# Kernel optimization log

Hardware: AMD Instinct MI355X
Metric: run time of the kernel (lower is better)

The kernel has to match this reference:

```python
import jax, jax.numpy as jnp
import numpy as np

K = 3  # hardcoded in DRKNN.__init__


def setup_inputs() -> dict:
    key = jax.random.key(0)
    k1, k2, k3 = jax.random.split(key, 3)
    N, Q, A, B = 100000, 1024, 8, 16
    dataTensorX = jax.random.normal(k1, (N, A, B), dtype=jnp.float32)
    dataTensorY = jax.random.normal(k2, (N, 3), dtype=jnp.float32)
    inputTensor = jax.random.normal(k3, (Q, A, B), dtype=jnp.float32)
    return {"dataTensorX": dataTensorX, "dataTensorY": dataTensorY, "inputTensor": inputTensor}


def reference(dataTensorX, dataTensorY, inputTensor):
    # Flatten feature dims (1,2) -> single feature axis F = A*B
    N = dataTensorX.shape[0]
    Q = inputTensor.shape[0]
    X = dataTensorX.reshape(N, -1)   # [N, F]
    Qf = inputTensor.reshape(Q, -1)  # [Q, F]
    # squared L2 distance via expansion: ||q||^2 - 2 q.x + ||x||^2 -> [Q, N]
    x2 = jnp.sum(X * X, axis=-1)     # [N]
    q2 = jnp.sum(Qf * Qf, axis=-1)   # [Q]
    dists = q2[:, None] - 2.0 * (Qf @ X.T) + x2[None, :]  # [Q, N]
    # k smallest distances == k largest of negated distances
    _, idx = jax.lax.top_k(-dists, K)  # idx: [Q, K] int32
    outs = dataTensorY[idx]            # [Q, K, label_dim]
    out = jnp.mean(outs, axis=1)       # [Q, label_dim]
    return out, idx
```

## Files before the change

kernel.cpp:

```cpp
#include <hip/hip_runtime.h>

#define F       128
#define TILE    128
#define NCHUNKS 64
#define KSTEP   32
#define TOPK    3
#define DINF    (__builtin_inff())
#define IMAX    0x7fffffff

typedef short short8 __attribute__((ext_vector_type(8)));
typedef float f32x4  __attribute__((ext_vector_type(4)));

__device__ __forceinline__ ushort f2bf(float f) {
    uint u = __float_as_uint(f);
    uint r = (u + 0x7fffu + ((u >> 16) & 1u)) >> 16;
    return (ushort)r;
}

__device__ __forceinline__ bool lex_less(float d1, int i1, float d2, int i2) {
    return (d1 < d2) || (d1 == d2 && i1 < i2);
}

__device__ __forceinline__ int slotOf(int n, int g, int s) {
    int gg = g ^ ((n >> 2) & 3);
    int ss = s ^ (n & 3);
    return (n * 4 + gg) * 4 + ss;
}

__device__ __forceinline__ void loadRows(const ushort* __restrict__ src, uint4* v, int t) {
    const int n = t & 127, half = t >> 7;
    const uint4* s4 = reinterpret_cast<const uint4*>(src + (size_t)n * F + half * 64);
    #pragma unroll
    for (int c = 0; c < 8; c++) v[c] = s4[c];
}
__device__ __forceinline__ void writeLDS(const uint4* v, uint4* sX16, int t) {
    const int n = t & 127, half = t >> 7;
    const uint* u = reinterpret_cast<const uint*>(v);
    #pragma unroll
    for (int sp = 0; sp < 2; sp++)
        #pragma unroll
        for (int g = 0; g < 4; g++) {
            int c0 = sp * 4 + (g >> 1);
            int i0 = (g & 1) * 2;
            uint4 slot = make_uint4(u[c0 * 4 + i0], u[c0 * 4 + i0 + 1],
                                    u[(c0 + 2) * 4 + i0], u[(c0 + 2) * 4 + i0 + 1]);
            sX16[slotOf(n, g, half * 2 + sp)] = slot;
        }
}


__global__ void conv_kernel(const float* __restrict__ src, ushort* __restrict__ dst,
                            float* __restrict__ nrm, int rows, int rowsPad) {
    int row  = blockIdx.x * 4 + (threadIdx.x >> 6);
    int lane = threadIdx.x & 63;
    if (row >= rowsPad) return;
    if (row < rows) {
        float2 v = *reinterpret_cast<const float2*>(&src[(size_t)row * F + lane * 2]);
        ushort2 b; b.x = f2bf(v.x); b.y = f2bf(v.y);
        *reinterpret_cast<ushort2*>(&dst[(size_t)row * F + lane * 2]) = b;
        float s = v.x * v.x + v.y * v.y;
        #pragma unroll
        for (int m = 32; m >= 1; m >>= 1) s += __shfl_xor(s, m, 64);
        if (lane == 0) nrm[row] = s;
    } else {
        *reinterpret_cast<ushort2*>(&dst[(size_t)row * F + lane * 2]) = make_ushort2(0, 0);
        if (lane == 0) nrm[row] = DINF;
    }
}

__global__ __launch_bounds__(256) void knn_p1(
    const ushort* __restrict__ Xbf, const ushort* __restrict__ Qbf,
    const float* __restrict__ x2f, float* __restrict__ part,
    int NTILES, int NSUB)
{
    __shared__ uint4 sX16[2048];
    __shared__ float sx2[TILE];

    const int t   = threadIdx.x;
    const int w   = t >> 6;
    const int l   = t & 63;
    const int l15 = l & 15;
    const int g   = l >> 4;
    const int chunk = blockIdx.x;
    const int qbase = blockIdx.y * TILE;
    const int tile0 = (int)(((long)chunk * NTILES) >> 6);
    const int tile1 = (int)(((long)(chunk + 1) * NTILES) >> 6);

    {
        uint4 qv[8];
        loadRows(Qbf + (size_t)qbase * F, qv, t);
        writeLDS(qv, sX16, t);
    }
    __syncthreads();
    short8 qf[2][4];
    #pragma unroll
    for (int fqi = 0; fqi < 2; fqi++)
        #pragma unroll
        for (int s = 0; s < 4; s++) {
            int qn = w * 32 + fqi * 16 + l15;
            qf[fqi][s] = *reinterpret_cast<const short8*>(&sX16[slotOf(qn, g, s)]);
        }

    uint4 v[8];
    loadRows(Xbf + (size_t)tile0 * TILE * F, v, t);

    for (int tile = tile0; tile < tile1; tile++) {
        __syncthreads();
        writeLDS(v, sX16, t);
        if (t < 32)
            *reinterpret_cast<float4*>(&sx2[t * 4]) =
                *reinterpret_cast<const float4*>(&x2f[tile * TILE + t * 4]);
        if (tile + 1 < tile1)
            loadRows(Xbf + (size_t)(tile + 1) * TILE * F, v, t);
        __syncthreads();

        f32x4 acc[8][2];
        #pragma unroll
        for (int fm = 0; fm < 8; fm++)
            #pragma unroll
            for (int fqi = 0; fqi < 2; fqi++)
                acc[fm][fqi] = (f32x4){0.f, 0.f, 0.f, 0.f};

        #pragma unroll
        for (int s = 0; s < 4; s++) {
            short8 af[8];
            #pragma unroll
            for (int fm = 0; fm < 8; fm++)
                af[fm] = *reinterpret_cast<const short8*>(&sX16[slotOf(fm * 16 + l15, g, s)]);
            #pragma unroll
            for (int fm = 0; fm < 8; fm++) {
                acc[fm][0] = __builtin_amdgcn_mfma_f32_16x16x32_bf16(af[fm], qf[0][s], acc[fm][0], 0, 0, 0);
                acc[fm][1] = __builtin_amdgcn_mfma_f32_16x16x32_bf16(af[fm], qf[1][s], acc[fm][1], 0, 0, 0);
            }
        }

        #pragma unroll
        for (int sb = 0; sb < 4; sb++) {
            float4 xa = *reinterpret_cast<const float4*>(&sx2[sb * 32 + g * 4]);
            float4 xb = *reinterpret_cast<const float4*>(&sx2[sb * 32 + 16 + g * 4]);
            #pragma unroll
            for (int fqi = 0; fqi < 2; fqi++) {
                f32x4 ca = acc[sb * 2][fqi];
                f32x4 cb = acc[sb * 2 + 1][fqi];
                float t0 = fmaf(-2.f, ca[0], xa.x), t1 = fmaf(-2.f, ca[1], xa.y);
                float t2 = fmaf(-2.f, ca[2], xa.z), t3 = fmaf(-2.f, ca[3], xa.w);
                float t4 = fmaf(-2.f, cb[0], xb.x), t5 = fmaf(-2.f, cb[1], xb.y);
                float t6 = fmaf(-2.f, cb[2], xb.z), t7 = fmaf(-2.f, cb[3], xb.w);
                float m = fminf(fminf(fminf(t0, t1), fminf(t2, t3)),
                                fminf(fminf(t4, t5), fminf(t6, t7)));
                m = fminf(m, __shfl_xor(m, 16, 64));
                m = fminf(m, __shfl_xor(m, 32, 64));
                if (g == 0)
                    part[(size_t)(qbase + w * 32 + fqi * 16 + l15) * NSUB + (tile * 4 + sb)] = m;
            }
        }
    }
}

__global__ __launch_bounds__(256) void knn_p2(
    const float* __restrict__ part, const float* __restrict__ Xf,
    const float* __restrict__ x2f, const float* __restrict__ Qf,
    const float* __restrict__ q2f, const float* __restrict__ Y,
    float* __restrict__ out, int NSUB, int qTotal, int Nreal)
{
    __shared__ float sq[4][F];
    __shared__ int   scnt[4];
    __shared__ int   slist[4][128];

    const int t = threadIdx.x, w = t >> 6, l = t & 63;
    const int q = blockIdx.x * 4 + w;

    *reinterpret_cast<float2*>(&sq[w][l * 2]) =
        *reinterpret_cast<const float2*>(&Qf[(size_t)q * F + l * 2]);
    if (l == 0) scnt[w] = 0;
    __syncthreads();

    const float q2v = q2f[q];
    const int iters = (NSUB + 63) / 64;
    const size_t prow = (size_t)q * NSUB;

    float a0 = DINF, a1 = DINF, a2 = DINF;
    for (int it = 0; it < iters; it++) {
        int i = it * 64 + l;
        float v = (i < NSUB) ? part[prow + i] : DINF;
        if (v < a2) { a2 = v;
            if (a2 < a1) { float x = a2; a2 = a1; a1 = x; }
            if (a1 < a0) { float x = a1; a1 = a0; a0 = x; } }
    }
    #pragma unroll
    for (int m = 1; m < 64; m <<= 1) {
        float o0 = __shfl_xor(a0, m, 64), o1 = __shfl_xor(a1, m, 64), o2 = __shfl_xor(a2, m, 64);
        #pragma unroll
        for (int c = 0; c < 3; c++) {
            float v = (c == 0) ? o0 : (c == 1) ? o1 : o2;
            if (v < a2) { a2 = v;
                if (a2 < a1) { float x = a2; a2 = a1; a1 = x; }
                if (a1 < a0) { float x = a1; a1 = a0; a0 = x; } }
        }
    }
    const float tau = a2 + 4.5f;

    for (int it = 0; it < iters; it++) {
        int i = it * 64 + l;
        float v = (i < NSUB) ? part[prow + i] : DINF;
        if (v <= tau) {
            int slot = atomicAdd(&scnt[w], 1);
            if (slot < 128) slist[w][slot] = i;
        }
    }
    __syncthreads();
    const int ncand = min(scnt[w], 128);

    float b0d = DINF, b1d = DINF, b2d = DINF;
    int   b0i = IMAX, b1i = IMAX, b2i = IMAX;
    auto ins = [&](float d, int ix) {
        if (lex_less(d, ix, b2d, b2i)) {
            b2d = d; b2i = ix;
            if (lex_less(b2d, b2i, b1d, b1i)) {
                float td = b2d; b2d = b1d; b1d = td; int ti = b2i; b2i = b1i; b1i = ti; }
            if (lex_less(b1d, b1i, b0d, b0i)) {
                float td = b1d; b1d = b0d; b0d = td; int ti = b1i; b1i = b0i; b0i = ti; }
        }
    };

    const int half = l >> 5, pl = l & 31;
    for (int ci = 0; ci < ncand; ci++) {
        int p = slist[w][ci] * 32 + pl;
        float s = 0.f;
        if (p < Nreal) {
            const float4* xr = reinterpret_cast<const float4*>(&Xf[(size_t)p * F + half * 64]);
            const float4* qr = reinterpret_cast<const float4*>(&sq[w][half * 64]);
            float s0 = 0.f, s1 = 0.f, s2 = 0.f, s3 = 0.f;
            #pragma unroll
            for (int j = 0; j < 16; j++) {
                float4 xv = xr[j], qv = qr[j];
                s0 = fmaf(xv.x, qv.x, s0); s1 = fmaf(xv.y, qv.y, s1);
                s2 = fmaf(xv.z, qv.z, s2); s3 = fmaf(xv.w, qv.w, s3);
            }
            s = (s0 + s1) + (s2 + s3);
        }
        s += __shfl_xor(s, 32, 64);
        if (l < 32 && p < Nreal) {
            float d = (q2v - 2.0f * s) + x2f[p];
            ins(d, p);
        }
    }

    #pragma unroll
    for (int m = 1; m < 64; m <<= 1) {
        float od0 = __shfl_xor(b0d, m, 64); int oi0 = __shfl_xor(b0i, m, 64);
        float od1 = __shfl_xor(b1d, m, 64); int oi1 = __shfl_xor(b1i, m, 64);
        float od2 = __shfl_xor(b2d, m, 64); int oi2 = __shfl_xor(b2i, m, 64);
        ins(od0, oi0); ins(od1, oi1); ins(od2, oi2);
    }

    if (l == 0) {
        int idx_off = qTotal * 3;
        #pragma unroll
        for (int c = 0; c < 3; c++) {
            float s = Y[(size_t)b0i * 3 + c] + Y[(size_t)b1i * 3 + c] + Y[(size_t)b2i * 3 + c];
            out[q * 3 + c] = s / 3.0f;
        }
        out[idx_off + q * 3 + 0] = (float)b0i;
        out[idx_off + q * 3 + 1] = (float)b1i;
        out[idx_off + q * 3 + 2] = (float)b2i;
    }
}


__global__ void fb_rownorm(const float* __restrict__ src, float* __restrict__ dst, int rows) {
    int row  = blockIdx.x * 4 + (threadIdx.x >> 6);
    int lane = threadIdx.x & 63;
    if (row >= rows) return;
    float2 v = *reinterpret_cast<const float2*>(&src[(size_t)row * F + lane * 2]);
    float s = v.x * v.x + v.y * v.y;
    #pragma unroll
    for (int m = 32; m >= 1; m >>= 1) s += __shfl_xor(s, m, 64);
    if (lane == 0) dst[row] = s;
}

__global__ __launch_bounds__(256) void fb_phase1(
    const float* __restrict__ X, const float* __restrict__ Qm,
    const float* __restrict__ x2, const float* __restrict__ q2,
    float* __restrict__ part_d, int* __restrict__ part_i,
    int N, int ntiles)
{
    __shared__ __align__(16) union {
        struct { float a[KSTEP * TILE]; float b[KSTEP * TILE]; } s;
        struct { float d[TILE][16][TOPK]; int i[TILE][16][TOPK]; } r;
    } u;

    const int t  = threadIdx.x;
    const int tx = t & 15;
    const int ty = t >> 4;
    const int chunk = blockIdx.x;
    const int qbase = blockIdx.y * TILE;
    const int ar0 = ty * 4;
    const int bc0 = tx * 4;
    const int srow0 = t >> 2;
    const int skc0  = t & 3;

    float t3d[8][TOPK];
    int   t3i[8][TOPK];
    #pragma unroll
    for (int i = 0; i < 8; i++)
        #pragma unroll
        for (int c = 0; c < TOPK; c++) { t3d[i][c] = DINF; t3i[i][c] = IMAX; }

    float q2r[8];
    #pragma unroll
    for (int i = 0; i < 8; i++) {
        int r = (i < 4) ? (ar0 + i) : (64 + ar0 + i - 4);
        q2r[i] = q2[qbase + r];
    }

    for (int tile = chunk; tile < ntiles; tile += NCHUNKS) {
        float acc[8][8];
        #pragma unroll
        for (int i = 0; i < 8; i++)
            #pragma unroll
            for (int j = 0; j < 8; j++) acc[i][j] = 0.0f;

        for (int ks = 0; ks < F; ks += KSTEP) {
            __syncthreads();
            #pragma unroll
            for (int lq = 0; lq < 4; lq++) {
                int row = srow0 | ((lq >> 1) << 6);
                int kc  = skc0 | ((lq & 1) << 2);
                int sw  = (kc & 3) << 3;
                int base = (kc * 4) * TILE + (row ^ sw);

                float4 va = *reinterpret_cast<const float4*>(
                    &Qm[(size_t)(qbase + row) * F + ks + kc * 4]);
                u.s.a[base + 0 * TILE] = va.x;
                u.s.a[base + 1 * TILE] = va.y;
                u.s.a[base + 2 * TILE] = va.z;
                u.s.a[base + 3 * TILE] = va.w;

                int n = tile * TILE + row;
                float4 vb = make_float4(0.f, 0.f, 0.f, 0.f);
                if (n < N) vb = *reinterpret_cast<const float4*>(
                    &X[(size_t)n * F + ks + kc * 4]);
                u.s.b[base + 0 * TILE] = vb.x;
                u.s.b[base + 1 * TILE] = vb.y;
                u.s.b[base + 2 * TILE] = vb.z;
                u.s.b[base + 3 * TILE] = vb.w;
            }
            __syncthreads();

            #pragma unroll
            for (int kk = 0; kk < KSTEP; kk++) {
                int sw = ((kk >> 2) & 3) << 3;
                float4 a0 = *reinterpret_cast<const float4*>(&u.s.a[kk * TILE + (ar0 ^ sw)]);
                float4 a1 = *reinterpret_cast<const float4*>(&u.s.a[kk * TILE + 64 + (ar0 ^ sw)]);
                float4 b0 = *reinterpret_cast<const float4*>(&u.s.b[kk * TILE + (bc0 ^ sw)]);
                float4 b1 = *reinterpret_cast<const float4*>(&u.s.b[kk * TILE + 64 + (bc0 ^ sw)]);
                float av[8] = {a0.x, a0.y, a0.z, a0.w, a1.x, a1.y, a1.z, a1.w};
                float bv[8] = {b0.x, b0.y, b0.z, b0.w, b1.x, b1.y, b1.z, b1.w};
                #pragma unroll
                for (int i = 0; i < 8; i++)
                    #pragma unroll
                    for (int j = 0; j < 8; j++)
                        acc[i][j] = fmaf(av[i], bv[j], acc[i][j]);
            }
        }

        #pragma unroll
        for (int j = 0; j < 8; j++) {
            int n = tile * TILE + ((j < 4) ? (bc0 + j) : (64 + bc0 + j - 4));
            if (n < N) {
                float xc = x2[n];
                #pragma unroll
                for (int i = 0; i < 8; i++) {
                    float d = (q2r[i] - 2.0f * acc[i][j]) + xc;
                    if (d < t3d[i][2]) {
                        t3d[i][2] = d; t3i[i][2] = n;
                        if (t3d[i][2] < t3d[i][1]) {
                            float td = t3d[i][2]; t3d[i][2] = t3d[i][1]; t3d[i][1] = td;
                            int ti = t3i[i][2]; t3i[i][2] = t3i[i][1]; t3i[i][1] = ti;
                        }
                        if (t3d[i][1] < t3d[i][0]) {
                            float td = t3d[i][1]; t3d[i][1] = t3d[i][0]; t3d[i][0] = td;
                            int ti = t3i[i][1]; t3i[i][1] = t3i[i][0]; t3i[i][0] = ti;
                        }
                    }
                }
            }
        }
    }

    __syncthreads();
    #pragma unroll
    for (int i = 0; i < 8; i++) {
        int r = (i < 4) ? (ar0 + i) : (64 + ar0 + i - 4);
        #pragma unroll
        for (int c = 0; c < TOPK; c++) {
            u.r.d[r][tx][c] = t3d[i][c];
            u.r.i[r][tx][c] = t3i[i][c];
        }
    }
    __syncthreads();

    if (t < TILE) {
        int row = t;
        float b0d = DINF, b1d = DINF, b2d = DINF;
        int   b0i = IMAX, b1i = IMAX, b2i = IMAX;
        for (int s = 0; s < 16; s++) {
            #pragma unroll
            for (int c = 0; c < TOPK; c++) {
                float d = u.r.d[row][s][c];
                int  ix = u.r.i[row][s][c];
                if (lex_less(d, ix, b2d, b2i)) {
                    b2d = d; b2i = ix;
                    if (lex_less(b2d, b2i, b1d, b1i)) {
                        float td = b2d; b2d = b1d; b1d = td;
                        int ti = b2i; b2i = b1i; b1i = ti;
                    }
                    if (lex_less(b1d, b1i, b0d, b0i)) {
                        float td = b1d; b1d = b0d; b0d = td;
                        int ti = b1i; b1i = b0i; b0i = ti;
                    }
                }
            }
        }
        size_t base = ((size_t)(qbase + row) * NCHUNKS + chunk) * TOPK;
        part_d[base + 0] = b0d; part_d[base + 1] = b1d; part_d[base + 2] = b2d;
        part_i[base + 0] = b0i; part_i[base + 1] = b1i; part_i[base + 2] = b2i;
    }
}

__global__ void fb_phase2(const float* __restrict__ part_d, const int* __restrict__ part_i,
                          const float* __restrict__ Y, float* __restrict__ out, int Q)
{
    int q    = blockIdx.x * 4 + (threadIdx.x >> 6);
    int lane = threadIdx.x & 63;
    if (q >= Q) return;

    float b0d = DINF, b1d = DINF, b2d = DINF;
    int   b0i = IMAX, b1i = IMAX, b2i = IMAX;

    auto ins = [&](float d, int ix) {
        if (lex_less(d, ix, b2d, b2i)) {
            b2d = d; b2i = ix;
            if (lex_less(b2d, b2i, b1d, b1i)) {
                float td = b2d; b2d = b1d; b1d = td;
                int ti = b2i; b2i = b1i; b1i = ti;
            }
            if (lex_less(b1d, b1i, b0d, b0i)) {
                float td = b1d; b1d = b0d; b0d = td;
                int ti = b1i; b1i = b0i; b0i = ti;
            }
        }
    };

    const int total = NCHUNKS * TOPK;
    size_t base = (size_t)q * total;
    for (int e = lane; e < total; e += 64)
        ins(part_d[base + e], part_i[base + e]);

    #pragma unroll
    for (int m = 1; m < 64; m <<= 1) {
        float od0 = __shfl_xor(b0d, m, 64); int oi0 = __shfl_xor(b0i, m, 64);
        float od1 = __shfl_xor(b1d, m, 64); int oi1 = __shfl_xor(b1i, m, 64);
        float od2 = __shfl_xor(b2d, m, 64); int oi2 = __shfl_xor(b2i, m, 64);
        ins(od0, oi0); ins(od1, oi1); ins(od2, oi2);
    }

    if (lane == 0) {
        int idx_off = Q * 3;
        #pragma unroll
        for (int c = 0; c < 3; c++) {
            float s = Y[(size_t)b0i * 3 + c] + Y[(size_t)b1i * 3 + c] + Y[(size_t)b2i * 3 + c];
            out[q * 3 + c] = s / 3.0f;
        }
        out[idx_off + q * 3 + 0] = (float)b0i;
        out[idx_off + q * 3 + 1] = (float)b1i;
        out[idx_off + q * 3 + 2] = (float)b2i;
    }
}


extern "C" void kernel_launch(void* const* d_in, const int* in_sizes, int n_in,
                              void* d_out, int out_size, void* d_ws, size_t ws_size,
                              hipStream_t stream) {
    const float* Xf = (const float*)d_in[0];
    const float* Y  = (const float*)d_in[1];
    const float* Qf = (const float*)d_in[2];
    int N = in_sizes[1] / 3;
    int Q = in_sizes[2] / F;
    int NTILES = (N + TILE - 1) / TILE;
    int NPAD   = NTILES * TILE;
    int NSUB   = NTILES * 4;
    char* ws = (char*)d_ws;
    (void)n_in; (void)out_size;

    size_t oA = 0;
    auto allocA = [&](size_t b) { size_t r = oA; oA = (oA + b + 255) & ~(size_t)255; return r; };
    size_t off_Xbf  = allocA((size_t)NPAD * F * 2);
    size_t off_Qbf  = allocA((size_t)Q * F * 2);
    size_t off_x2   = allocA((size_t)NPAD * 4);
    size_t off_q2   = allocA((size_t)Q * 4);
    size_t off_part = allocA((size_t)NSUB * Q * 4);

    if (oA <= ws_size) {
        ushort* Xbf  = (ushort*)(ws + off_Xbf);
        ushort* Qbf  = (ushort*)(ws + off_Qbf);
        float*  x2f  = (float*) (ws + off_x2);
        float*  q2f  = (float*) (ws + off_q2);
        float*  part = (float*) (ws + off_part);

        hipLaunchKernelGGL(conv_kernel, dim3(NPAD / 4), dim3(256), 0, stream, Xf, Xbf, x2f, N, NPAD);
        hipLaunchKernelGGL(conv_kernel, dim3(Q / 4),    dim3(256), 0, stream, Qf, Qbf, q2f, Q, Q);
        hipLaunchKernelGGL(knn_p1, dim3(NCHUNKS, Q / TILE), dim3(256), 0, stream,
                           Xbf, Qbf, x2f, part, NTILES, NSUB);
        hipLaunchKernelGGL(knn_p2, dim3(Q / 4), dim3(256), 0, stream,
                           part, Xf, x2f, Qf, q2f, Y, (float*)d_out, NSUB, Q, N);
    } else {
        size_t oB = 0;
        auto allocB = [&](size_t b) { size_t r = oB; oB = (oB + b + 255) & ~(size_t)255; return r; };
        float* x2     = (float*)(ws + allocB((size_t)N * 4));
        float* q2     = (float*)(ws + allocB((size_t)Q * 4));
        float* part_d = (float*)(ws + allocB((size_t)Q * NCHUNKS * TOPK * 4));
        int*   part_i = (int*)  (ws + allocB((size_t)Q * NCHUNKS * TOPK * 4));

        hipLaunchKernelGGL(fb_rownorm, dim3((N + 3) / 4), dim3(256), 0, stream, Xf, x2, N);
        hipLaunchKernelGGL(fb_rownorm, dim3((Q + 3) / 4), dim3(256), 0, stream, Qf, q2, Q);
        hipLaunchKernelGGL(fb_phase1, dim3(NCHUNKS, Q / TILE), dim3(256), 0, stream,
                           Xf, Qf, x2, q2, part_d, part_i, N, NTILES);
        hipLaunchKernelGGL(fb_phase2, dim3((Q + 3) / 4), dim3(256), 0, stream,
                           part_d, part_i, Y, (float*)d_out, Q);
    }
}
```

Baseline: 136.6 us.

## Assign one query per block in knn_p2 with shared partial-min staging

Reworks the second pass so that each 256-thread block handles a single query instead of four queries with one wave each. The query's sub-tile minima are staged once into LDS. All four waves then cooperatively find the threshold, build a shared candidate list of up to 256 entries, split the exact-distance rescoring between them, and merge their top-3 through LDS. This aims to cut the serial per-wave candidate loop and the doubled global reads of the partials, at the cost of four times more blocks, extra block-wide syncs and about 14KB of LDS per block.

```diff
diff --git a/kernel.cpp b/kernel.cpp
--- a/kernel.cpp
+++ b/kernel.cpp
@@ -5,6 +5,7 @@
 #define NCHUNKS 64
 #define KSTEP   32
 #define TOPK    3
+#define NSUB_MAX 3200
 #define DINF    (__builtin_inff())
 #define IMAX    0x7fffffff
 
@@ -163,26 +164,29 @@
     const float* __restrict__ q2f, const float* __restrict__ Y,
     float* __restrict__ out, int NSUB, int qTotal, int Nreal)
 {
-    __shared__ float sq[4][F];
-    __shared__ int   scnt[4];
-    __shared__ int   slist[4][128];
+    __shared__ float spart[NSUB_MAX];
+    __shared__ float sq[F];
+    __shared__ float rd3[4][3];
+    __shared__ int   scnt;
+    __shared__ int   slist[256];
+    __shared__ float wrd[4][3];
+    __shared__ int   wri[4][3];
 
     const int t = threadIdx.x, w = t >> 6, l = t & 63;
-    const int q = blockIdx.x * 4 + w;
-
-    *reinterpret_cast<float2*>(&sq[w][l * 2]) =
-        *reinterpret_cast<const float2*>(&Qf[(size_t)q * F + l * 2]);
-    if (l == 0) scnt[w] = 0;
-    __syncthreads();
-
-    const float q2v = q2f[q];
-    const int iters = (NSUB + 63) / 64;
+    const int q = blockIdx.x;
+
+    if (t < 64)
+        *reinterpret_cast<float2*>(&sq[t * 2]) =
+            *reinterpret_cast<const float2*>(&Qf[(size_t)q * F + t * 2]);
+    if (t == 0) scnt = 0;
+
     const size_t prow = (size_t)q * NSUB;
+    for (int i = t; i < NSUB; i += 256) spart[i] = part[prow + i];
+    __syncthreads();
 
     float a0 = DINF, a1 = DINF, a2 = DINF;
-    for (int it = 0; it < iters; it++) {
-        int i = it * 64 + l;
-        float v = (i < NSUB) ? part[prow + i] : DINF;
+    for (int i = t; i < NSUB; i += 256) {
+        float v = spart[i];
         if (v < a2) { a2 = v;
             if (a2 < a1) { float x = a2; a2 = a1; a1 = x; }
             if (a1 < a0) { float x = a1; a1 = a0; a0 = x; } }
@@ -198,18 +202,33 @@
                 if (a1 < a0) { float x = a1; a1 = a0; a0 = x; } }
         }
     }
-    const float tau = a2 + 4.5f;
-
-    for (int it = 0; it < iters; it++) {
-        int i = it * 64 + l;
-        float v = (i < NSUB) ? part[prow + i] : DINF;
-        if (v <= tau) {
-            int slot = atomicAdd(&scnt[w], 1);
-            if (slot < 128) slist[w][slot] = i;
-        }
-    }
-    __syncthreads();
-    const int ncand = min(scnt[w], 128);
+    if (l == 0) { rd3[w][0] = a0; rd3[w][1] = a1; rd3[w][2] = a2; }
+    __syncthreads();
+
+    float tau;
+    {
+        float c0 = DINF, c1 = DINF, c2 = DINF;
+        #pragma unroll
+        for (int ww = 0; ww < 4; ww++)
+            #pragma unroll
+            for (int c = 0; c < 3; c++) {
+                float v = rd3[ww][c];
+                if (v < c2) { c2 = v;
+                    if (c2 < c1) { float x = c2; c2 = c1; c1 = x; }
+                    if (c1 < c0) { float x = c1; c1 = c0; c0 = x; } }
+            }
+        tau = c2 + 4.5f;
+    }
+
+    for (int i = t; i < NSUB; i += 256) {
+        if (spart[i] <= tau) {
+            int slot = atomicAdd(&scnt, 1);
+            if (slot < 256) slist[slot] = i;
+        }
+    }
+    __syncthreads();
+    const int ncand = min(scnt, 256);
+    const float q2v = q2f[q];
 
     float b0d = DINF, b1d = DINF, b2d = DINF;
     int   b0i = IMAX, b1i = IMAX, b2i = IMAX;
@@ -224,12 +243,12 @@
     };
 
     const int half = l >> 5, pl = l & 31;
-    for (int ci = 0; ci < ncand; ci++) {
-        int p = slist[w][ci] * 32 + pl;
+    for (int ci = w; ci < ncand; ci += 4) {
+        int p = slist[ci] * 32 + pl;
         float s = 0.f;
         if (p < Nreal) {
             const float4* xr = reinterpret_cast<const float4*>(&Xf[(size_t)p * F + half * 64]);
-            const float4* qr = reinterpret_cast<const float4*>(&sq[w][half * 64]);
+            const float4* qr = reinterpret_cast<const float4*>(&sq[half * 64]);
             float s0 = 0.f, s1 = 0.f, s2 = 0.f, s3 = 0.f;
             #pragma unroll
             for (int j = 0; j < 16; j++) {
@@ -253,8 +272,18 @@
         float od2 = __shfl_xor(b2d, m, 64); int oi2 = __shfl_xor(b2i, m, 64);
         ins(od0, oi0); ins(od1, oi1); ins(od2, oi2);
     }
-
     if (l == 0) {
+        wrd[w][0] = b0d; wrd[w][1] = b1d; wrd[w][2] = b2d;
+        wri[w][0] = b0i; wri[w][1] = b1i; wri[w][2] = b2i;
+    }
+    __syncthreads();
+
+    if (t == 0) {
+        #pragma unroll
+        for (int ww = 1; ww < 4; ww++)
+            #pragma unroll
+            for (int c = 0; c < 3; c++)
+                ins(wrd[ww][c], wri[ww][c]);
         int idx_off = qTotal * 3;
         #pragma unroll
         for (int c = 0; c < 3; c++) {
@@ -502,7 +531,7 @@
     size_t off_q2   = allocA((size_t)Q * 4);
     size_t off_part = allocA((size_t)NSUB * Q * 4);
 
-    if (oA <= ws_size) {
+    if (oA <= ws_size && NSUB <= NSUB_MAX) {
         ushort* Xbf  = (ushort*)(ws + off_Xbf);
         ushort* Qbf  = (ushort*)(ws + off_Qbf);
         float*  x2f  = (float*) (ws + off_x2);
@@ -513,7 +542,7 @@
         hipLaunchKernelGGL(conv_kernel, dim3(Q / 4),    dim3(256), 0, stream, Qf, Qbf, q2f, Q, Q);
         hipLaunchKernelGGL(knn_p1, dim3(NCHUNKS, Q / TILE), dim3(256), 0, stream,
                            Xbf, Qbf, x2f, part, NTILES, NSUB);
-        hipLaunchKernelGGL(knn_p2, dim3(Q / 4), dim3(256), 0, stream,
+        hipLaunchKernelGGL(knn_p2, dim3(Q), dim3(256), 0, stream,
                            part, Xf, x2f, Qf, q2f, Y, (float*)d_out, NSUB, Q, N);
     } else {
         size_t oB = 0;
```

Measured after the change: 116.9 us. 14.4% less time.
